# Kernel optimization log

Hardware: AMD Instinct MI355X
Metric: run time of the kernel (lower is better)

Reference implementation:

```python
import jax, jax.numpy as jnp
import numpy as np

# SH constants (standard 3DGS eval_sh, degree 3)
C0 = 0.28209479177387814
C1 = 0.4886025119029199
C2 = (1.0925484305920792, -1.0925484305920792, 0.31539156525252005, -1.0925484305920792, 0.5462742152960396)
C3 = (-0.5900435899266435, 2.890611442640554, -0.4570457994644658, 0.3731763325901154, -0.4570457994644658, 1.445305721320277, -0.5900435899266435)

N_GAUSS = 4096
N_PTS = 32768
CHUNK = 4096  # math-identical to torch's 16384 chunking (pure concat of independent points)


def quat_to_rot(q):
    # q: (N,4) normalized, (w,x,y,z) as in 3DGS build_rotation
    r, x, y, z = q[:, 0], q[:, 1], q[:, 2], q[:, 3]
    R = jnp.stack([
        jnp.stack([1 - 2 * (y * y + z * z), 2 * (x * y - r * z), 2 * (x * z + r * y)], -1),
        jnp.stack([2 * (x * y + r * z), 1 - 2 * (x * x + z * z), 2 * (y * z - r * x)], -1),
        jnp.stack([2 * (x * z - r * y), 2 * (y * z + r * x), 1 - 2 * (x * x + y * y)], -1),
    ], axis=-2)  # (N,3,3)
    return R


def eval_sh3(sh, dirs):
    # sh: (N,16) scalar SH coeffs; dirs: (C,N,3) unit directions -> (C,N)
    x, y, z = dirs[..., 0], dirs[..., 1], dirs[..., 2]
    xx, yy, zz = x * x, y * y, z * z
    xy, yz, xz = x * y, y * z, x * z
    s = sh[None]  # (1,N,16)
    res = C0 * s[..., 0]
    res = res - C1 * y * s[..., 1] + C1 * z * s[..., 2] - C1 * x * s[..., 3]
    res = (res + C2[0] * xy * s[..., 4] + C2[1] * yz * s[..., 5]
           + C2[2] * (2 * zz - xx - yy) * s[..., 6]
           + C2[3] * xz * s[..., 7] + C2[4] * (xx - yy) * s[..., 8])
    res = (res + C3[0] * y * (3 * xx - yy) * s[..., 9] + C3[1] * xy * z * s[..., 10]
           + C3[2] * y * (4 * zz - xx - yy) * s[..., 11]
           + C3[3] * z * (2 * zz - 3 * xx - 3 * yy) * s[..., 12]
           + C3[4] * x * (4 * zz - xx - yy) * s[..., 13]
           + C3[5] * z * (xx - yy) * s[..., 14]
           + C3[6] * x * (xx - yy - 3 * zz) * s[..., 15])
    return res


def setup_inputs() -> dict:
    key = jax.random.key(0)
    ks = jax.random.split(key, 9)
    return {
        "network_pts": jax.random.normal(ks[0], (N_PTS, 3), jnp.float32),
        "network_view": jax.random.normal(ks[1], (N_PTS, 3), jnp.float32),
        "network_tx": jax.random.normal(ks[2], (N_PTS, 3), jnp.float32),
        "xyz": jax.random.normal(ks[3], (N_GAUSS, 3), jnp.float32),
        "sh_dc": jax.random.normal(ks[4], (N_GAUSS, 1), jnp.float32),
        "sh_rest": 0.1 * jax.random.normal(ks[5], (N_GAUSS, 15), jnp.float32),
        "scaling": jnp.float32(-3.0) + 0.2 * jax.random.normal(ks[6], (N_GAUSS, 3), jnp.float32),
        "rotation": jax.random.normal(ks[7], (N_GAUSS, 4), jnp.float32),
        "opacity_logit": jax.random.normal(ks[8], (N_GAUSS, 1), jnp.float32),
    }


def reference(network_pts, network_view, network_tx, xyz, sh_dc, sh_rest, scaling, rotation, opacity_logit):
    # activations, matching GaussianModel.setup_functions
    sh = jnp.concatenate([sh_dc, sh_rest], axis=1)            # (N,16)
    s = jnp.exp(scaling)                                      # (N,3)
    q = rotation / jnp.linalg.norm(rotation, axis=1, keepdims=True)
    R = quat_to_rot(q)                                        # (N,3,3)
    # precision = (L L^T)^{-1} with L = R diag(s)  =>  R diag(1/s^2) R^T
    prec = jnp.einsum('nij,nj,nkj->nik', R, 1.0 / (s * s), R)  # (N,3,3)
    op = jax.nn.sigmoid(opacity_logit)[:, 0]                  # (N,)

    pts = network_pts.reshape(-1, CHUNK, 3)

    def chunk_fn(p):  # p: (C,3)
        diff = p[:, None, :] - xyz[None, :, :]                # (C,N,3)
        maha = jnp.einsum('cni,nij,cnj->cn', diff, prec, diff)
        w = op[None, :] * jnp.exp(-0.5 * maha)                # (C,N)
        # dir_pp = xyz - query_point, normalized (as in get_magnitude)
        dirs = -diff / jnp.linalg.norm(diff, axis=-1, keepdims=True)
        mag = jnp.maximum(eval_sh3(sh, dirs), 0.0)            # (C,N)
        return w.sum(axis=1), (w * mag).sum(axis=1)

    opac_c, sig_c = jax.lax.map(chunk_fn, pts)
    return opac_c.reshape(-1), sig_c.reshape(-1)
```

## Files before the change

### kernel.cpp

```cpp
#include <hip/hip_runtime.h>
#include <hip/hip_bf16.h>

#define N_GAUSS 4096
#define N_PTS   32768
#define BLOCK   256
#define NSPLIT  64
#define SEGSZ   (N_GAUSS / NSPLIT)
#define NBLK_PT 128
#define GSTRIDE 28
#define NCELL   4096

#define SH_C0  0.28209479177387814f
#define SH_C1  0.4886025119029199f

#define WS_GP     0
#define WS_GHIST  114688
#define WS_CELLID 118784
#define WS_SPTS   151552
#define WS_ACC    282624

__device__ __forceinline__ int cell_of(float x, float y, float z) {
    int cx = min(15, max(0, (int)((x + 3.2f) * 2.5f)));
    int cy = min(15, max(0, (int)((y + 3.2f) * 2.5f)));
    int cz = min(15, max(0, (int)((z + 3.2f) * 2.5f)));
    int ex = (cx & 1) | ((cx & 2) << 2) | ((cx & 4) << 4) | ((cx & 8) << 6);
    int ey = (cy & 1) | ((cy & 2) << 2) | ((cy & 4) << 4) | ((cy & 8) << 6);
    int ez = (cz & 1) | ((cz & 2) << 2) | ((cz & 4) << 4) | ((cz & 8) << 6);
    return ex | (ey << 1) | (ez << 2);
}

__global__ __launch_bounds__(1024) void setup_kernel(
    const float* __restrict__ pts, const float* __restrict__ xyz,
    const float* __restrict__ sh_dc, const float* __restrict__ sh_rest,
    const float* __restrict__ scaling, const float* __restrict__ rotation,
    const float* __restrict__ opl, float* __restrict__ gp,
    int* __restrict__ cellid, int* __restrict__ ghist, float* __restrict__ acc)
{
    const int t = threadIdx.x, bx = blockIdx.x;

    if (bx >= 5) {
        float4* a4 = (float4*)acc;
        int base = (bx - 5) * 1024 * 8 + t;
        #pragma unroll
        for (int i = 0; i < 8; ++i) a4[base + i * 1024] = make_float4(0.f, 0.f, 0.f, 0.f);
        return;
    }
    if (bx > 0) {
        int g = (bx - 1) * 1024 + t;
        float s0 = scaling[3*g+0], s1 = scaling[3*g+1], s2 = scaling[3*g+2];
        float i0 = __expf(-2.0f * s0);
        float i1 = __expf(-2.0f * s1);
        float i2 = __expf(-2.0f * s2);
        float maxs2 = __expf(2.0f * fmaxf(s0, fmaxf(s1, s2)));

        float r = rotation[4*g+0], x = rotation[4*g+1];
        float y = rotation[4*g+2], z = rotation[4*g+3];
        float n = rsqrtf(r*r + x*x + y*y + z*z);
        r *= n; x *= n; y *= n; z *= n;
        float R00 = 1.f - 2.f*(y*y + z*z), R01 = 2.f*(x*y - r*z), R02 = 2.f*(x*z + r*y);
        float R10 = 2.f*(x*y + r*z), R11 = 1.f - 2.f*(x*x + z*z), R12 = 2.f*(y*z - r*x);
        float R20 = 2.f*(x*z - r*y), R21 = 2.f*(y*z + r*x), R22 = 1.f - 2.f*(x*x + y*y);

        float pxx = 0.5f*(R00*R00*i0 + R01*R01*i1 + R02*R02*i2);
        float pxy = 0.5f*(R00*R10*i0 + R01*R11*i1 + R02*R12*i2);
        float pxz = 0.5f*(R00*R20*i0 + R01*R21*i1 + R02*R22*i2);
        float pyy = 0.5f*(R10*R10*i0 + R11*R11*i1 + R12*R12*i2);
        float pyz = 0.5f*(R10*R20*i0 + R11*R21*i1 + R12*R22*i2);
        float pzz = 0.5f*(R20*R20*i0 + R21*R21*i1 + R22*R22*i2);

        float op   = 1.f / (1.f + __expf(-opl[g]));
        float lnop = __logf(op);
        float Tg   = 2.0f * maxs2 * (lnop + 16.0f);

        float* G = gp + (size_t)g * GSTRIDE;
        G[0] = xyz[3*g+0]; G[1] = xyz[3*g+1]; G[2] = xyz[3*g+2]; G[3] = Tg;
        G[4] = pxx; G[5] = pxy; G[6] = pxz; G[7] = pyy; G[8] = pyz; G[9] = pzz;
        G[10] = lnop; G[11] = 0.f;

        const float* sr = sh_rest + (size_t)g * 15;
        G[12] =  SH_C0 * sh_dc[g];
        G[13] = -SH_C1 * sr[0];
        G[14] =  SH_C1 * sr[1];
        G[15] = -SH_C1 * sr[2];
        G[16] =  1.0925484305920792f  * sr[3];
        G[17] = -1.0925484305920792f  * sr[4];
        G[18] =  0.31539156525252005f * sr[5];
        G[19] = -1.0925484305920792f  * sr[6];
        G[20] =  0.5462742152960396f  * sr[7];
        G[21] = -0.5900435899266435f  * sr[8];
        G[22] =  2.890611442640554f   * sr[9];
        G[23] = -0.4570457994644658f  * sr[10];
        G[24] =  0.3731763325901154f  * sr[11];
        G[25] = -0.4570457994644658f  * sr[12];
        G[26] =  1.445305721320277f   * sr[13];
        G[27] = -0.5900435899266435f  * sr[14];
        return;
    }

    __shared__ int s_hist[NCELL];
    __shared__ int s_scan[1024];
    #pragma unroll
    for (int i = 0; i < 4; ++i) s_hist[t + i * 1024] = 0;
    __syncthreads();
    for (int p = t; p < N_PTS; p += 1024) {
        float x = pts[3*p+0], y = pts[3*p+1], z = pts[3*p+2];
        int cell = cell_of(x, y, z);
        cellid[p] = cell;
        atomicAdd(&s_hist[cell], 1);
    }
    __syncthreads();
    int b = t * 4;
    int c0 = s_hist[b], c1 = s_hist[b+1], c2 = s_hist[b+2], c3 = s_hist[b+3];
    int s = c0 + c1 + c2 + c3;
    s_scan[t] = s;
    __syncthreads();
    for (int off = 1; off < 1024; off <<= 1) {
        int v = (t >= off) ? s_scan[t - off] : 0;
        __syncthreads();
        s_scan[t] += v;
        __syncthreads();
    }
    int excl = s_scan[t] - s;
    ghist[b]   = excl;
    ghist[b+1] = excl + c0;
    ghist[b+2] = excl + c0 + c1;
    ghist[b+3] = excl + c0 + c1 + c2;
}

__global__ __launch_bounds__(256) void scatter_kernel(
    const float* __restrict__ pts, const int* __restrict__ cellid,
    int* __restrict__ ghist, float4* __restrict__ spts)
{
    int p = blockIdx.x * 256 + threadIdx.x;
    float x = pts[3*p+0], y = pts[3*p+1], z = pts[3*p+2];
    int pos = atomicAdd(&ghist[cellid[p]], 1);
    spts[pos] = make_float4(x, y, z, __int_as_float(p));
}

__device__ __forceinline__ void eval_one(
    const float* __restrict__ G, float dx, float dy, float dz, float d2,
    float& opac, float& sig)
{
    float vx = G[4]*dx + G[5]*dy + G[6]*dz;
    float vy = G[5]*dx + G[7]*dy + G[8]*dz;
    float vz = G[6]*dx + G[8]*dy + G[9]*dz;
    float maha = dx*vx + dy*vy + dz*vz;
    float w = __expf(G[10] - maha);
    opac += w;

    if (__any(w > 1e-9f)) {
        float rinv = rsqrtf(d2);
        float x = -dx * rinv, y = -dy * rinv, z = -dz * rinv;
        float xx = x*x, yy = y*y, zz = z*z;
        float xy = x*y, yz = y*z, xz = x*z;

        float res = G[12];
        res += y * G[13];
        res += z * G[14];
        res += x * G[15];
        res += xy * G[16];
        res += yz * G[17];
        res += (3.f*zz - 1.f) * G[18];
        res += xz * G[19];
        float xxmyy = xx - yy;
        res += xxmyy * G[20];
        res += y * (3.f*xx - yy) * G[21];
        res += (xy * z) * G[22];
        float f5z1 = 5.f*zz - 1.f;
        res += y * f5z1 * G[23];
        res += z * (5.f*zz - 3.f) * G[24];
        res += x * f5z1 * G[25];
        res += z * xxmyy * G[26];
        res += x * (xxmyy - 3.f*zz) * G[27];

        sig += w * fmaxf(res, 0.f);
    }
}

__global__ __launch_bounds__(BLOCK, 4) void gauss_kernel(
    const float4* __restrict__ spts, const float* __restrict__ gp,
    float* __restrict__ acc)
{
    __shared__ float s_min[4][3], s_max[4][3];
    __shared__ int s_nact;
    __shared__ int s_act[SEGSZ];

    const int tid = threadIdx.x;
    const int pb  = blockIdx.x;
    const int seg = blockIdx.y;
    float4 P = spts[pb * 256 + tid];
    const float px = P.x, py = P.y, pz = P.z;

    float mnx = px, mxx = px, mny = py, mxy = py, mnz = pz, mxz = pz;
    #pragma unroll
    for (int off = 32; off >= 1; off >>= 1) {
        mnx = fminf(mnx, __shfl_xor(mnx, off));
        mxx = fmaxf(mxx, __shfl_xor(mxx, off));
        mny = fminf(mny, __shfl_xor(mny, off));
        mxy = fmaxf(mxy, __shfl_xor(mxy, off));
        mnz = fminf(mnz, __shfl_xor(mnz, off));
        mxz = fmaxf(mxz, __shfl_xor(mxz, off));
    }
    const int wave = tid >> 6;
    if ((tid & 63) == 0) {
        s_min[wave][0] = mnx; s_min[wave][1] = mny; s_min[wave][2] = mnz;
        s_max[wave][0] = mxx; s_max[wave][1] = mxy; s_max[wave][2] = mxz;
    }
    if (tid == 0) s_nact = 0;
    __syncthreads();
    const float bmnx = fminf(fminf(s_min[0][0], s_min[1][0]), fminf(s_min[2][0], s_min[3][0]));
    const float bmny = fminf(fminf(s_min[0][1], s_min[1][1]), fminf(s_min[2][1], s_min[3][1]));
    const float bmnz = fminf(fminf(s_min[0][2], s_min[1][2]), fminf(s_min[2][2], s_min[3][2]));
    const float bmxx = fmaxf(fmaxf(s_max[0][0], s_max[1][0]), fmaxf(s_max[2][0], s_max[3][0]));
    const float bmxy = fmaxf(fmaxf(s_max[0][1], s_max[1][1]), fmaxf(s_max[2][1], s_max[3][1]));
    const float bmxz = fmaxf(fmaxf(s_max[0][2], s_max[1][2]), fmaxf(s_max[2][2], s_max[3][2]));

    if (tid < SEGSZ) {
        const int gg = seg * SEGSZ + tid;
        const float* Gc = gp + (size_t)gg * GSTRIDE;
        float cx = Gc[0], cy = Gc[1], cz = Gc[2], Tg = Gc[3];
        float ddx = fmaxf(0.f, fmaxf(bmnx - cx, cx - bmxx));
        float ddy = fmaxf(0.f, fmaxf(bmny - cy, cy - bmxy));
        float ddz = fmaxf(0.f, fmaxf(bmnz - cz, cz - bmxz));
        float dd2 = ddx*ddx + ddy*ddy + ddz*ddz;
        if (dd2 <= Tg) {
            int slot = atomicAdd(&s_nact, 1);
            s_act[slot] = gg;
        }
    }
    __syncthreads();
    const int nact = s_nact;
    if (nact == 0) return;

    float opac = 0.f, sig = 0.f;
    for (int j = 0; j < nact; j += 2) {
        const bool has1 = (j + 1 < nact);
        const int g0 = __builtin_amdgcn_readfirstlane(s_act[j]);
        const int g1 = __builtin_amdgcn_readfirstlane(s_act[has1 ? j + 1 : j]);
        const float* __restrict__ A = gp + (size_t)g0 * GSTRIDE;
        const float* __restrict__ B = gp + (size_t)g1 * GSTRIDE;

        float a0 = A[0], a1 = A[1], a2 = A[2], aT = A[3];
        float b0 = B[0], b1 = B[1], b2 = B[2], bT = B[3];
        float adx = px - a0, ady = py - a1, adz = pz - a2;
        float bdx = px - b0, bdy = py - b1, bdz = pz - b2;
        float ad2 = adx*adx + ady*ady + adz*adz;
        float bd2 = bdx*bdx + bdy*bdy + bdz*bdz;

        if (!__all(ad2 > aT)) eval_one(A, adx, ady, adz, ad2, opac, sig);
        if (has1 && !__all(bd2 > bT)) eval_one(B, bdx, bdy, bdz, bd2, opac, sig);
    }

    const int pos = pb * 256 + tid;
    atomicAdd(&acc[pos], opac);
    atomicAdd(&acc[N_PTS + pos], sig);
}

__global__ __launch_bounds__(256) void permute_kernel(
    const float* __restrict__ acc, const float4* __restrict__ spts,
    float* __restrict__ out)
{
    int p = blockIdx.x * 256 + threadIdx.x;
    int orig = __float_as_int(spts[p].w);
    out[orig] = acc[p];
    out[N_PTS + orig] = acc[N_PTS + p];
}

extern "C" void kernel_launch(void* const* d_in, const int* in_sizes, int n_in,
                              void* d_out, int out_size, void* d_ws, size_t ws_size,
                              hipStream_t stream) {
    const float* pts      = (const float*)d_in[0];
    const float* xyz      = (const float*)d_in[3];
    const float* sh_dc    = (const float*)d_in[4];
    const float* sh_rest  = (const float*)d_in[5];
    const float* scaling  = (const float*)d_in[6];
    const float* rotation = (const float*)d_in[7];
    const float* opl      = (const float*)d_in[8];

    float*  out    = (float*)d_out;
    float*  wsf    = (float*)d_ws;
    float*  gp     = wsf + WS_GP;
    int*    ghist  = (int*)(wsf + WS_GHIST);
    int*    cellid = (int*)(wsf + WS_CELLID);
    float4* spts   = (float4*)(wsf + WS_SPTS);
    float*  acc    = wsf + WS_ACC;

    setup_kernel<<<dim3(7), dim3(1024), 0, stream>>>(
        pts, xyz, sh_dc, sh_rest, scaling, rotation, opl, gp, cellid, ghist, acc);
    scatter_kernel<<<dim3(NBLK_PT), dim3(256), 0, stream>>>(pts, cellid, ghist, spts);

    dim3 grid(NBLK_PT, NSPLIT);
    gauss_kernel<<<grid, dim3(BLOCK), 0, stream>>>(spts, gp, acc);
    permute_kernel<<<dim3(NBLK_PT), dim3(256), 0, stream>>>(acc, spts, out);
}
```

Before: 128.6 us.

## Split gaussian culling into separate kernel and balance compacted lists across blocks

Moves the per-point-block bounding-box culling out of the main kernel into a new cull kernel that writes a compacted list of candidate gaussians per block to workspace. The main kernel then splits each compacted list into 32-entry chunks strided across 16 y-blocks, so work is spread by surviving gaussian count rather than fixed 64-gaussian segments. Blocks whose segments had no survivors no longer launch the full reduction prologue. The cost is one extra kernel launch, a global list of up to 4096 ints per point block, and global instead of shared-memory list reads. Occupancy hint rises to 8 blocks per CU.

```diff
diff --git a/kernel.cpp b/kernel.cpp
--- a/kernel.cpp
+++ b/kernel.cpp
@@ -3,12 +3,11 @@
 
 #define N_GAUSS 4096
 #define N_PTS   32768
-#define BLOCK   256
-#define NSPLIT  64
-#define SEGSZ   (N_GAUSS / NSPLIT)
 #define NBLK_PT 128
 #define GSTRIDE 28
 #define NCELL   4096
+#define CHUNK   32
+#define GY      16
 
 #define SH_C0  0.28209479177387814f
 #define SH_C1  0.4886025119029199f
@@ -18,6 +17,8 @@
 #define WS_CELLID 118784
 #define WS_SPTS   151552
 #define WS_ACC    282624
+#define WS_GCOUNT 348160
+#define WS_GLIST  348416
 
 __device__ __forceinline__ int cell_of(float x, float y, float z) {
     int cx = min(15, max(0, (int)((x + 3.2f) * 2.5f)));
@@ -137,6 +138,59 @@
     spts[pos] = make_float4(x, y, z, __int_as_float(p));
 }
 
+__global__ __launch_bounds__(256) void cull_kernel(
+    const float4* __restrict__ spts, const float* __restrict__ gp,
+    int* __restrict__ glist, int* __restrict__ gcount)
+{
+    __shared__ float s_min[4][3], s_max[4][3];
+    __shared__ int s_n;
+
+    const int tid = threadIdx.x, pb = blockIdx.x;
+    float4 P = spts[pb * 256 + tid];
+    float px = P.x, py = P.y, pz = P.z;
+
+    float mnx = px, mxx = px, mny = py, mxy = py, mnz = pz, mxz = pz;
+    #pragma unroll
+    for (int off = 32; off >= 1; off >>= 1) {
+        mnx = fminf(mnx, __shfl_xor(mnx, off));
+        mxx = fmaxf(mxx, __shfl_xor(mxx, off));
+        mny = fminf(mny, __shfl_xor(mny, off));
+        mxy = fmaxf(mxy, __shfl_xor(mxy, off));
+        mnz = fminf(mnz, __shfl_xor(mnz, off));
+        mxz = fmaxf(mxz, __shfl_xor(mxz, off));
+    }
+    const int wave = tid >> 6;
+    if ((tid & 63) == 0) {
+        s_min[wave][0] = mnx; s_min[wave][1] = mny; s_min[wave][2] = mnz;
+        s_max[wave][0] = mxx; s_max[wave][1] = mxy; s_max[wave][2] = mxz;
+    }
+    if (tid == 0) s_n = 0;
+    __syncthreads();
+    const float bmnx = fminf(fminf(s_min[0][0], s_min[1][0]), fminf(s_min[2][0], s_min[3][0]));
+    const float bmny = fminf(fminf(s_min[0][1], s_min[1][1]), fminf(s_min[2][1], s_min[3][1]));
+    const float bmnz = fminf(fminf(s_min[0][2], s_min[1][2]), fminf(s_min[2][2], s_min[3][2]));
+    const float bmxx = fmaxf(fmaxf(s_max[0][0], s_max[1][0]), fmaxf(s_max[2][0], s_max[3][0]));
+    const float bmxy = fmaxf(fmaxf(s_max[0][1], s_max[1][1]), fmaxf(s_max[2][1], s_max[3][1]));
+    const float bmxz = fmaxf(fmaxf(s_max[0][2], s_max[1][2]), fmaxf(s_max[2][2], s_max[3][2]));
+
+    int* list = glist + (size_t)pb * N_GAUSS;
+    #pragma unroll 4
+    for (int i = 0; i < 16; ++i) {
+        const int g = i * 256 + tid;
+        const float4 c = *(const float4*)(gp + (size_t)g * GSTRIDE);
+        float ddx = fmaxf(0.f, fmaxf(bmnx - c.x, c.x - bmxx));
+        float ddy = fmaxf(0.f, fmaxf(bmny - c.y, c.y - bmxy));
+        float ddz = fmaxf(0.f, fmaxf(bmnz - c.z, c.z - bmxz));
+        float dd2 = ddx*ddx + ddy*ddy + ddz*ddz;
+        if (dd2 <= c.w) {
+            int slot = atomicAdd(&s_n, 1);
+            list[slot] = g;
+        }
+    }
+    __syncthreads();
+    if (tid == 0) gcount[pb] = s_n;
+}
+
 __device__ __forceinline__ void eval_one(
     const float* __restrict__ G, float dx, float dy, float dz, float d2,
     float& opac, float& sig)
@@ -177,78 +231,41 @@
     }
 }
 
-__global__ __launch_bounds__(BLOCK, 4) void gauss_kernel(
+__global__ __launch_bounds__(256, 8) void gauss_kernel(
     const float4* __restrict__ spts, const float* __restrict__ gp,
+    const int* __restrict__ glist, const int* __restrict__ gcount,
     float* __restrict__ acc)
 {
-    __shared__ float s_min[4][3], s_max[4][3];
-    __shared__ int s_nact;
-    __shared__ int s_act[SEGSZ];
-
     const int tid = threadIdx.x;
     const int pb  = blockIdx.x;
-    const int seg = blockIdx.y;
+    const int by  = blockIdx.y;
+    const int count = gcount[pb];
+    if (by * CHUNK >= count) return;
+
     float4 P = spts[pb * 256 + tid];
     const float px = P.x, py = P.y, pz = P.z;
-
-    float mnx = px, mxx = px, mny = py, mxy = py, mnz = pz, mxz = pz;
-    #pragma unroll
-    for (int off = 32; off >= 1; off >>= 1) {
-        mnx = fminf(mnx, __shfl_xor(mnx, off));
-        mxx = fmaxf(mxx, __shfl_xor(mxx, off));
-        mny = fminf(mny, __shfl_xor(mny, off));
-        mxy = fmaxf(mxy, __shfl_xor(mxy, off));
-        mnz = fminf(mnz, __shfl_xor(mnz, off));
-        mxz = fmaxf(mxz, __shfl_xor(mxz, off));
-    }
-    const int wave = tid >> 6;
-    if ((tid & 63) == 0) {
-        s_min[wave][0] = mnx; s_min[wave][1] = mny; s_min[wave][2] = mnz;
-        s_max[wave][0] = mxx; s_max[wave][1] = mxy; s_max[wave][2] = mxz;
-    }
-    if (tid == 0) s_nact = 0;
-    __syncthreads();
-    const float bmnx = fminf(fminf(s_min[0][0], s_min[1][0]), fminf(s_min[2][0], s_min[3][0]));
-    const float bmny = fminf(fminf(s_min[0][1], s_min[1][1]), fminf(s_min[2][1], s_min[3][1]));
-    const float bmnz = fminf(fminf(s_min[0][2], s_min[1][2]), fminf(s_min[2][2], s_min[3][2]));
-    const float bmxx = fmaxf(fmaxf(s_max[0][0], s_max[1][0]), fmaxf(s_max[2][0], s_max[3][0]));
-    const float bmxy = fmaxf(fmaxf(s_max[0][1], s_max[1][1]), fmaxf(s_max[2][1], s_max[3][1]));
-    const float bmxz = fmaxf(fmaxf(s_max[0][2], s_max[1][2]), fmaxf(s_max[2][2], s_max[3][2]));
-
-    if (tid < SEGSZ) {
-        const int gg = seg * SEGSZ + tid;
-        const float* Gc = gp + (size_t)gg * GSTRIDE;
-        float cx = Gc[0], cy = Gc[1], cz = Gc[2], Tg = Gc[3];
-        float ddx = fmaxf(0.f, fmaxf(bmnx - cx, cx - bmxx));
-        float ddy = fmaxf(0.f, fmaxf(bmny - cy, cy - bmxy));
-        float ddz = fmaxf(0.f, fmaxf(bmnz - cz, cz - bmxz));
-        float dd2 = ddx*ddx + ddy*ddy + ddz*ddz;
-        if (dd2 <= Tg) {
-            int slot = atomicAdd(&s_nact, 1);
-            s_act[slot] = gg;
+    const int* __restrict__ list = glist + (size_t)pb * N_GAUSS;
+
+    float opac = 0.f, sig = 0.f;
+    for (int j0 = by * CHUNK; j0 < count; j0 += GY * CHUNK) {
+        const int jend = min(j0 + CHUNK, count);
+        for (int j = j0; j < jend; j += 2) {
+            const bool has1 = (j + 1 < jend);
+            const int g0 = __builtin_amdgcn_readfirstlane(list[j]);
+            const int g1 = __builtin_amdgcn_readfirstlane(list[has1 ? j + 1 : j]);
+            const float* __restrict__ A = gp + (size_t)g0 * GSTRIDE;
+            const float* __restrict__ B = gp + (size_t)g1 * GSTRIDE;
+
+            float a0 = A[0], a1 = A[1], a2 = A[2], aT = A[3];
+            float b0 = B[0], b1 = B[1], b2 = B[2], bT = B[3];
+            float adx = px - a0, ady = py - a1, adz = pz - a2;
+            float bdx = px - b0, bdy = py - b1, bdz = pz - b2;
+            float ad2 = adx*adx + ady*ady + adz*adz;
+            float bd2 = bdx*bdx + bdy*bdy + bdz*bdz;
+
+            if (!__all(ad2 > aT)) eval_one(A, adx, ady, adz, ad2, opac, sig);
+            if (has1 && !__all(bd2 > bT)) eval_one(B, bdx, bdy, bdz, bd2, opac, sig);
         }
-    }
-    __syncthreads();
-    const int nact = s_nact;
-    if (nact == 0) return;
-
-    float opac = 0.f, sig = 0.f;
-    for (int j = 0; j < nact; j += 2) {
-        const bool has1 = (j + 1 < nact);
-        const int g0 = __builtin_amdgcn_readfirstlane(s_act[j]);
-        const int g1 = __builtin_amdgcn_readfirstlane(s_act[has1 ? j + 1 : j]);
-        const float* __restrict__ A = gp + (size_t)g0 * GSTRIDE;
-        const float* __restrict__ B = gp + (size_t)g1 * GSTRIDE;
-
-        float a0 = A[0], a1 = A[1], a2 = A[2], aT = A[3];
-        float b0 = B[0], b1 = B[1], b2 = B[2], bT = B[3];
-        float adx = px - a0, ady = py - a1, adz = pz - a2;
-        float bdx = px - b0, bdy = py - b1, bdz = pz - b2;
-        float ad2 = adx*adx + ady*ady + adz*adz;
-        float bd2 = bdx*bdx + bdy*bdy + bdz*bdz;
-
-        if (!__all(ad2 > aT)) eval_one(A, adx, ady, adz, ad2, opac, sig);
-        if (has1 && !__all(bd2 > bT)) eval_one(B, bdx, bdy, bdz, bd2, opac, sig);
     }
 
     const int pos = pb * 256 + tid;
@@ -284,12 +301,15 @@
     int*    cellid = (int*)(wsf + WS_CELLID);
     float4* spts   = (float4*)(wsf + WS_SPTS);
     float*  acc    = wsf + WS_ACC;
+    int*    gcount = (int*)(wsf + WS_GCOUNT);
+    int*    glist  = (int*)(wsf + WS_GLIST);
 
     setup_kernel<<<dim3(7), dim3(1024), 0, stream>>>(
         pts, xyz, sh_dc, sh_rest, scaling, rotation, opl, gp, cellid, ghist, acc);
     scatter_kernel<<<dim3(NBLK_PT), dim3(256), 0, stream>>>(pts, cellid, ghist, spts);
-
-    dim3 grid(NBLK_PT, NSPLIT);
-    gauss_kernel<<<grid, dim3(BLOCK), 0, stream>>>(spts, gp, acc);
+    cull_kernel<<<dim3(NBLK_PT), dim3(256), 0, stream>>>(spts, gp, glist, gcount);
+
+    gauss_kernel<<<dim3(NBLK_PT, GY), dim3(256), 0, stream>>>(
+        spts, gp, glist, gcount, acc);
     permute_kernel<<<dim3(NBLK_PT), dim3(256), 0, stream>>>(acc, spts, out);
 }
```

New measurement: 173.6 us. 35.0% more time.
